# Optimization experiments

Hardware: AMD Instinct MI355X
Metric: run time of the kernel (lower is better)

## Reference

```python
import math
import jax, jax.numpy as jnp
import numpy as np

NUM_HEADS = 16

def setup_inputs() -> dict:
    key = jax.random.key(0)
    k1, k2, k3, k4, k5 = jax.random.split(key, 5)
    B, S, D = 8, 4096, 1024
    x = jax.random.normal(k1, (B, S, D), dtype=jnp.float32)
    W_qkv = jax.random.normal(k2, (D, 3 * D), dtype=jnp.float32) * (1.0 / math.sqrt(D))
    b_qkv = jax.random.normal(k3, (3 * D,), dtype=jnp.float32) * 0.02
    W_out = jax.random.normal(k4, (D, D), dtype=jnp.float32) * (1.0 / math.sqrt(D))
    b_out = jax.random.normal(k5, (D,), dtype=jnp.float32) * 0.02
    return {"x": x, "W_qkv": W_qkv, "b_qkv": b_qkv, "W_out": W_out, "b_out": b_out}

def reference(x, W_qkv, b_qkv, W_out, b_out):
    B, S, D = x.shape
    H = NUM_HEADS
    hd = D // H
    scale = 1.0 / math.sqrt(hd)
    # QKV projection: (B,S,D) -> (B,S,3D), reshaped to (B,S,H,3*hd)
    qkv = (x @ W_qkv + b_qkv).reshape(B, S, H, 3 * hd)
    q, k, v = jnp.split(qkv, 3, axis=-1)  # each (B,S,H,hd)
    # Faithful to source: no head permute, so attention is across the H heads
    # at each (batch, seq) position. scores: (B,S,H,H)
    scores = jnp.einsum('bsqd,bskd->bsqk', q, k) * scale
    attn = jax.nn.softmax(scores, axis=-1)
    values = jnp.einsum('bsqk,bskd->bsqd', attn, v).reshape(B, S, D)
    return values @ W_out + b_out
```

## Files before the change

kernel.cpp:

```cpp
#include <hip/hip_runtime.h>
#include <hip/hip_bf16.h>

#define TOKENS   32768
#define DMODEL   1024
#define THREE_D  3072

using u16 = unsigned short;
typedef __attribute__((ext_vector_type(8))) short short8;
typedef __attribute__((ext_vector_type(4))) float f32x4;

__device__ __forceinline__ float bf2f(u16 u) {
  union { unsigned int i; float f; } v; v.i = ((unsigned int)u) << 16; return v.f;
}
__device__ __forceinline__ u16 f2bf(float f) {
  __hip_bfloat16 h = __float2bfloat16(f);
  return *reinterpret_cast<u16*>(&h);
}

__device__ __forceinline__ void gload_lds16(const u16* g, u16* l) {
  __builtin_amdgcn_global_load_lds((const __attribute__((address_space(1))) void*)g,
                                   (__attribute__((address_space(3))) void*)l,
                                   16, 0, 0);
}

__global__ __launch_bounds__(256) void convert_f32_bf16(const float* __restrict__ in,
                                                        u16* __restrict__ out, long n) {
  long i = ((long)blockIdx.x * 256 + threadIdx.x) * 4;
  if (i >= n) return;
  float4 v = *reinterpret_cast<const float4*>(in + i);
  ushort4 o;
  o.x = f2bf(v.x); o.y = f2bf(v.y); o.z = f2bf(v.z); o.w = f2bf(v.w);
  *reinterpret_cast<ushort4*>(out + i) = o;
}

__global__ __launch_bounds__(256) void transpose_convert(const float* __restrict__ in,
                                                         u16* __restrict__ out,
                                                         int R, int C) {
  __shared__ u16 tile[32][33];
  const int bc = blockIdx.x * 32;
  const int br = blockIdx.y * 32;
  const int tx = threadIdx.x & 31;
  const int ty = threadIdx.x >> 5;
  #pragma unroll
  for (int i = 0; i < 32; i += 8)
    tile[ty + i][tx] = f2bf(in[(long)(br + ty + i) * C + bc + tx]);
  __syncthreads();
  #pragma unroll
  for (int i = 0; i < 32; i += 8)
    out[(long)(bc + ty + i) * R + br + tx] = tile[tx][ty + i];
}

#define BM 128
#define BN 128
#define BK 64

template <bool OUT_F32>
__global__ __launch_bounds__(256) void gemm_bt_bias(
    const u16* __restrict__ A, const u16* __restrict__ BT,
    const float* __restrict__ bias, void* __restrict__ Cv,
    int M, int N, int K, long a_stride, int a_grp) {
  __shared__ alignas(16) u16 As[BM * BK];
  __shared__ alignas(16) u16 Bs[BN * BK];

  const int tiles_n = N / BN;
  const int bm = (blockIdx.x / tiles_n) * BM;
  const int bn = (blockIdx.x % tiles_n) * BN;
  const int tid  = threadIdx.x;
  const int wave = tid >> 6;
  const int lane = tid & 63;
  const int wm   = (wave & 1) * 64;
  const int wn   = (wave >> 1) * 64;
  const int lrow = lane & 15;
  const int quad = lane >> 4;

  const int sr     = lane >> 3;
  const int schunk = (lane & 7) ^ sr;
  const int scol   = schunk * 8;

  f32x4 acc[4][4];
  #pragma unroll
  for (int i = 0; i < 4; i++)
    #pragma unroll
    for (int j = 0; j < 4; j++) acc[i][j] = (f32x4){0.f, 0.f, 0.f, 0.f};

  for (int k0 = 0; k0 < K; k0 += BK) {
    const long aoff = (long)(k0 >> 6) * a_grp + scol;
    __syncthreads();
    #pragma unroll
    for (int r = 0; r < 4; r++) {
      const int row = wave * 32 + r * 8 + sr;
      gload_lds16(A  + (long)(bm + row) * a_stride + aoff, As + (wave * 32 + r * 8) * BK);
      gload_lds16(BT + (long)(bn + row) * K + k0 + scol,  Bs + (wave * 32 + r * 8) * BK);
    }
    __syncthreads();

    #pragma unroll
    for (int kh = 0; kh < 2; kh++) {
      const int xs = lrow & 7;
      short8 a[4], b[4];
      #pragma unroll
      for (int mi = 0; mi < 4; mi++)
        a[mi] = *reinterpret_cast<const short8*>(
            &As[(wm + mi * 16 + lrow) * BK + (((kh * 4 + quad) ^ xs) * 8)]);
      #pragma unroll
      for (int ni = 0; ni < 4; ni++)
        b[ni] = *reinterpret_cast<const short8*>(
            &Bs[(wn + ni * 16 + lrow) * BK + (((kh * 4 + quad) ^ xs) * 8)]);
      #pragma unroll
      for (int mi = 0; mi < 4; mi++)
        #pragma unroll
        for (int ni = 0; ni < 4; ni++)
          acc[mi][ni] = __builtin_amdgcn_mfma_f32_16x16x32_bf16(a[mi], b[ni], acc[mi][ni], 0, 0, 0);
    }
  }

  #pragma unroll
  for (int ni = 0; ni < 4; ni++) {
    const int col = bn + wn + ni * 16 + lrow;
    const float bv = bias[col];
    #pragma unroll
    for (int mi = 0; mi < 4; mi++) {
      #pragma unroll
      for (int r = 0; r < 4; r++) {
        const int row = bm + wm + mi * 16 + (lane >> 4) * 4 + r;
        const float val = acc[mi][ni][r] + bv;
        if (OUT_F32)
          ((float*)Cv)[(long)row * N + col] = val;
        else
          ((u16*)Cv)[(long)row * N + col] = f2bf(val);
      }
    }
  }
}

__global__ __launch_bounds__(256) void attn_local(u16* __restrict__ qkv) {
  __shared__ float p_s[4][16][16];
  const int tid  = threadIdx.x;
  const int wave = tid >> 6;
  const int lane = tid & 63;
  const int t    = blockIdx.x * 4 + wave;
  u16* row = qkv + (long)t * THREE_D;
  const int lrow = lane & 15;
  const int quad = lane >> 4;
  const int kq   = quad * 8;

  short8 a0 = *reinterpret_cast<const short8*>(row + lrow * 192 + kq);
  short8 a1 = *reinterpret_cast<const short8*>(row + lrow * 192 + 32 + kq);
  short8 b0 = *reinterpret_cast<const short8*>(row + lrow * 192 + 64 + kq);
  short8 b1 = *reinterpret_cast<const short8*>(row + lrow * 192 + 96 + kq);
  f32x4 s = {0.f, 0.f, 0.f, 0.f};
  s = __builtin_amdgcn_mfma_f32_16x16x32_bf16(a0, b0, s, 0, 0, 0);
  s = __builtin_amdgcn_mfma_f32_16x16x32_bf16(a1, b1, s, 0, 0, 0);

  const float scale = 0.125f;
  float p[4];
  #pragma unroll
  for (int r = 0; r < 4; r++) {
    float x = s[r] * scale;
    float m = x;
    #pragma unroll
    for (int mask = 1; mask < 16; mask <<= 1) m = fmaxf(m, __shfl_xor(m, mask));
    float e = __expf(x - m);
    float l = e;
    #pragma unroll
    for (int mask = 1; mask < 16; mask <<= 1) l += __shfl_xor(l, mask);
    p[r] = e / l;
  }
  #pragma unroll
  for (int r = 0; r < 4; r++) p_s[wave][quad * 4 + r][lrow] = p[r];
  __syncthreads();

  float o[16];
  #pragma unroll
  for (int i = 0; i < 16; i++) o[i] = 0.f;
  #pragma unroll
  for (int j = 0; j < 16; j++) {
    float vj = bf2f(row[j * 192 + 128 + lane]);
    #pragma unroll
    for (int i = 0; i < 16; i++) o[i] += p_s[wave][i][j] * vj;
  }
  #pragma unroll
  for (int i = 0; i < 16; i++)
    row[i * 192 + lane] = f2bf(o[i]);
}

extern "C" void kernel_launch(void* const* d_in, const int* in_sizes, int n_in,
                              void* d_out, int out_size, void* d_ws, size_t ws_size,
                              hipStream_t stream) {
  const float* x     = (const float*)d_in[0];
  const float* W_qkv = (const float*)d_in[1];
  const float* b_qkv = (const float*)d_in[2];
  const float* W_out = (const float*)d_in[3];
  const float* b_out = (const float*)d_in[4];
  float* out = (float*)d_out;

  char* ws = (char*)d_ws;
  u16* qkv   = (u16*)ws;  ws += (size_t)TOKENS * THREE_D * 2;
  u16* x_bf  = (u16*)ws;  ws += (size_t)TOKENS * DMODEL * 2;
  u16* wqkvT = (u16*)ws;  ws += (size_t)THREE_D * DMODEL * 2;
  u16* woutT = (u16*)ws;

  dim3 tb(256);
  convert_f32_bf16<<<dim3((TOKENS * DMODEL) / 1024), tb, 0, stream>>>(
      x, x_bf, (long)TOKENS * DMODEL);
  transpose_convert<<<dim3(THREE_D / 32, DMODEL / 32), tb, 0, stream>>>(W_qkv, wqkvT, DMODEL, THREE_D);
  transpose_convert<<<dim3(DMODEL / 32, DMODEL / 32), tb, 0, stream>>>(W_out, woutT, DMODEL, DMODEL);
  gemm_bt_bias<false><<<dim3((TOKENS / BM) * (THREE_D / BN)), tb, 0, stream>>>(
      x_bf, wqkvT, b_qkv, qkv, TOKENS, THREE_D, DMODEL, (long)DMODEL, 64);
  attn_local<<<dim3(TOKENS / 4), tb, 0, stream>>>(qkv);
  gemm_bt_bias<true><<<dim3((TOKENS / BM) * (DMODEL / BN)), tb, 0, stream>>>(
      qkv, woutT, b_out, out, TOKENS, DMODEL, DMODEL, (long)THREE_D, 192);
}
```

Measured before the change: 643.3 us.

## Rewrite GEMM as 256x256 double-buffered 8-wave pipelined kernel with XCD remap

Replaces the 128x128 single-buffered GEMM with a 256x256 tile computed by 512 threads. It uses double-buffered LDS and splits each k-step into quadrant phases, staging the next half-tiles while MFMAs run, with explicit vmcnt waits, barriers and setprio. It also remaps block IDs across the 8 XCDs for better L2 locality. The aim is to hide global-load latency and raise data reuse per tile, at the cost of more LDS use, more registers and fragile hand-ordered synchronisation.

```diff
diff --git a/kernel.cpp b/kernel.cpp
--- a/kernel.cpp
+++ b/kernel.cpp
@@ -50,84 +50,147 @@
     out[(long)(bc + ty + i) * R + br + tx] = tile[tx][ty + i];
 }
 
-#define BM 128
-#define BN 128
+#define BM 256
+#define BN 256
 #define BK 64
 
+#define VM4 asm volatile("s_waitcnt vmcnt(4)" ::: "memory")
+#define VM0 asm volatile("s_waitcnt vmcnt(0)" ::: "memory")
+#define VMN ((void)0)
+#define NOSTAGE ((void)0)
+
+#define STAGE_A(T, H)                                                          \
+  { _Pragma("unroll") for (int j_ = 0; j_ < 2; j_++) {                         \
+      const int lr_ = (H) * 128 + (wave * 2 + j_) * 8;                         \
+      gload_lds16(A + (long)(bm + lr_ + sr) * a_stride + (long)(T) * a_grp + scol, \
+                  &As[(T) & 1][lr_ * BK]);                                     \
+  } }
+#define STAGE_B(T, H)                                                          \
+  { _Pragma("unroll") for (int j_ = 0; j_ < 2; j_++) {                         \
+      const int lr_ = (H) * 128 + (wave * 2 + j_) * 8;                         \
+      gload_lds16(BT + (long)(bn + lr_ + sr) * K + (T) * BK + scol,            \
+                  &Bs[(T) & 1][lr_ * BK]);                                     \
+  } }
+
+#define PHASE(BUF, QR, QC, RDA, STAGE, VMW)                                    \
+  {                                                                            \
+    if (RDA) {                                                                 \
+      _Pragma("unroll") for (int mi = 0; mi < 2; mi++)                         \
+        _Pragma("unroll") for (int kh = 0; kh < 2; kh++)                       \
+          a[mi][kh] = *reinterpret_cast<const short8*>(                        \
+              &As[BUF][((QR) * 128 + wrow + mi * 16 + lrow) * BK +             \
+                       (((kh * 4 + quad) ^ xs) * 8)]);                         \
+    }                                                                          \
+    short8 b[4][2];                                                            \
+    _Pragma("unroll") for (int ni = 0; ni < 4; ni++)                           \
+      _Pragma("unroll") for (int kh = 0; kh < 2; kh++)                         \
+        b[ni][kh] = *reinterpret_cast<const short8*>(                          \
+            &Bs[BUF][((QC) * 128 + wcol + ni * 16 + lrow) * BK +               \
+                     (((kh * 4 + quad) ^ xs) * 8)]);                           \
+    STAGE;                                                                     \
+    VMW;                                                                       \
+    __builtin_amdgcn_s_barrier();                                              \
+    asm volatile("s_waitcnt lgkmcnt(0)" ::: "memory");                         \
+    __builtin_amdgcn_sched_barrier(0);                                         \
+    __builtin_amdgcn_s_setprio(1);                                             \
+    _Pragma("unroll") for (int mi = 0; mi < 2; mi++)                           \
+      _Pragma("unroll") for (int ni = 0; ni < 4; ni++) {                       \
+        acc[QR][QC][mi][ni] = __builtin_amdgcn_mfma_f32_16x16x32_bf16(         \
+            a[mi][0], b[ni][0], acc[QR][QC][mi][ni], 0, 0, 0);                 \
+        acc[QR][QC][mi][ni] = __builtin_amdgcn_mfma_f32_16x16x32_bf16(         \
+            a[mi][1], b[ni][1], acc[QR][QC][mi][ni], 0, 0, 0);                 \
+      }                                                                        \
+    __builtin_amdgcn_s_setprio(0);                                             \
+    __builtin_amdgcn_s_barrier();                                              \
+    __builtin_amdgcn_sched_barrier(0);                                         \
+  }
+
 template <bool OUT_F32>
-__global__ __launch_bounds__(256) void gemm_bt_bias(
+__global__ __launch_bounds__(512, 2) void gemm_bt_bias(
     const u16* __restrict__ A, const u16* __restrict__ BT,
     const float* __restrict__ bias, void* __restrict__ Cv,
     int M, int N, int K, long a_stride, int a_grp) {
-  __shared__ alignas(16) u16 As[BM * BK];
-  __shared__ alignas(16) u16 Bs[BN * BK];
-
+  __shared__ alignas(16) u16 As[2][BM * BK];
+  __shared__ alignas(16) u16 Bs[2][BN * BK];
+  (void)M;
+
+  const int cpx = gridDim.x >> 3;
+  const int wg  = ((int)blockIdx.x & 7) * cpx + ((int)blockIdx.x >> 3);
   const int tiles_n = N / BN;
-  const int bm = (blockIdx.x / tiles_n) * BM;
-  const int bn = (blockIdx.x % tiles_n) * BN;
+  const int bm = (wg / tiles_n) * BM;
+  const int bn = (wg % tiles_n) * BN;
+
   const int tid  = threadIdx.x;
   const int wave = tid >> 6;
   const int lane = tid & 63;
-  const int wm   = (wave & 1) * 64;
-  const int wn   = (wave >> 1) * 64;
+  const int wrow = (wave & 3) * 32;
+  const int wcol = (wave >> 2) * 64;
   const int lrow = lane & 15;
   const int quad = lane >> 4;
+  const int xs   = lrow & 7;
 
   const int sr     = lane >> 3;
   const int schunk = (lane & 7) ^ sr;
   const int scol   = schunk * 8;
 
-  f32x4 acc[4][4];
-  #pragma unroll
-  for (int i = 0; i < 4; i++)
-    #pragma unroll
-    for (int j = 0; j < 4; j++) acc[i][j] = (f32x4){0.f, 0.f, 0.f, 0.f};
-
-  for (int k0 = 0; k0 < K; k0 += BK) {
-    const long aoff = (long)(k0 >> 6) * a_grp + scol;
-    __syncthreads();
-    #pragma unroll
-    for (int r = 0; r < 4; r++) {
-      const int row = wave * 32 + r * 8 + sr;
-      gload_lds16(A  + (long)(bm + row) * a_stride + aoff, As + (wave * 32 + r * 8) * BK);
-      gload_lds16(BT + (long)(bn + row) * K + k0 + scol,  Bs + (wave * 32 + r * 8) * BK);
-    }
-    __syncthreads();
-
-    #pragma unroll
-    for (int kh = 0; kh < 2; kh++) {
-      const int xs = lrow & 7;
-      short8 a[4], b[4];
+  const int NT = K / BK;
+
+  f32x4 acc[2][2][2][4];
+  #pragma unroll
+  for (int i = 0; i < 2; i++)
+    #pragma unroll
+    for (int j = 0; j < 2; j++)
       #pragma unroll
-      for (int mi = 0; mi < 4; mi++)
-        a[mi] = *reinterpret_cast<const short8*>(
-            &As[(wm + mi * 16 + lrow) * BK + (((kh * 4 + quad) ^ xs) * 8)]);
+      for (int m = 0; m < 2; m++)
+        #pragma unroll
+        for (int n = 0; n < 4; n++) acc[i][j][m][n] = (f32x4){0.f, 0.f, 0.f, 0.f};
+
+  STAGE_A(0, 0); STAGE_A(0, 1); STAGE_B(0, 0); STAGE_B(0, 1);
+  STAGE_A(1, 0); STAGE_B(1, 1);
+  VM4;
+  __builtin_amdgcn_s_barrier();
+
+  short8 a[2][2];
+  #pragma unroll 1
+  for (int t = 0; t + 2 < NT; t += 2) {
+    PHASE(0, 0, 0, 1, STAGE_A(t + 1, 1), VMN);
+    PHASE(0, 0, 1, 0, STAGE_B(t + 1, 0), VMN);
+    PHASE(0, 1, 1, 1, STAGE_A(t + 2, 0), VMN);
+    PHASE(0, 1, 0, 0, STAGE_B(t + 2, 1), VM4);
+    PHASE(1, 0, 0, 1, STAGE_A(t + 2, 1), VMN);
+    PHASE(1, 0, 1, 0, STAGE_B(t + 2, 0), VMN);
+    PHASE(1, 1, 1, 1, STAGE_A(t + 3, 0), VMN);
+    PHASE(1, 1, 0, 0, STAGE_B(t + 3, 1), VM4);
+  }
+  PHASE(0, 0, 0, 1, STAGE_A(NT - 1, 1), VMN);
+  PHASE(0, 0, 1, 0, STAGE_B(NT - 1, 0), VMN);
+  PHASE(0, 1, 1, 1, NOSTAGE, VMN);
+  PHASE(0, 1, 0, 0, NOSTAGE, VM0);
+  PHASE(1, 0, 0, 1, NOSTAGE, VMN);
+  PHASE(1, 0, 1, 0, NOSTAGE, VMN);
+  PHASE(1, 1, 1, 1, NOSTAGE, VMN);
+  PHASE(1, 1, 0, 0, NOSTAGE, VMN);
+
+  #pragma unroll
+  for (int qc = 0; qc < 2; qc++) {
+    #pragma unroll
+    for (int ni = 0; ni < 4; ni++) {
+      const int col = bn + qc * 128 + wcol + ni * 16 + lrow;
+      const float bv = bias[col];
       #pragma unroll
-      for (int ni = 0; ni < 4; ni++)
-        b[ni] = *reinterpret_cast<const short8*>(
-            &Bs[(wn + ni * 16 + lrow) * BK + (((kh * 4 + quad) ^ xs) * 8)]);
-      #pragma unroll
-      for (int mi = 0; mi < 4; mi++)
+      for (int qr = 0; qr < 2; qr++) {
         #pragma unroll
-        for (int ni = 0; ni < 4; ni++)
-          acc[mi][ni] = __builtin_amdgcn_mfma_f32_16x16x32_bf16(a[mi], b[ni], acc[mi][ni], 0, 0, 0);
-    }
-  }
-
-  #pragma unroll
-  for (int ni = 0; ni < 4; ni++) {
-    const int col = bn + wn + ni * 16 + lrow;
-    const float bv = bias[col];
-    #pragma unroll
-    for (int mi = 0; mi < 4; mi++) {
-      #pragma unroll
-      for (int r = 0; r < 4; r++) {
-        const int row = bm + wm + mi * 16 + (lane >> 4) * 4 + r;
-        const float val = acc[mi][ni][r] + bv;
-        if (OUT_F32)
-          ((float*)Cv)[(long)row * N + col] = val;
-        else
-          ((u16*)Cv)[(long)row * N + col] = f2bf(val);
+        for (int mi = 0; mi < 2; mi++) {
+          #pragma unroll
+          for (int r = 0; r < 4; r++) {
+            const int row = bm + qr * 128 + wrow + mi * 16 + quad * 4 + r;
+            const float val = acc[qr][qc][mi][ni][r] + bv;
+            if (OUT_F32)
+              ((float*)Cv)[(long)row * N + col] = val;
+            else
+              ((u16*)Cv)[(long)row * N + col] = f2bf(val);
+          }
+        }
       }
     }
   }
@@ -201,13 +264,14 @@
   u16* woutT = (u16*)ws;
 
   dim3 tb(256);
+  dim3 gtb(512);
   convert_f32_bf16<<<dim3((TOKENS * DMODEL) / 1024), tb, 0, stream>>>(
       x, x_bf, (long)TOKENS * DMODEL);
   transpose_convert<<<dim3(THREE_D / 32, DMODEL / 32), tb, 0, stream>>>(W_qkv, wqkvT, DMODEL, THREE_D);
   transpose_convert<<<dim3(DMODEL / 32, DMODEL / 32), tb, 0, stream>>>(W_out, woutT, DMODEL, DMODEL);
-  gemm_bt_bias<false><<<dim3((TOKENS / BM) * (THREE_D / BN)), tb, 0, stream>>>(
+  gemm_bt_bias<false><<<dim3((TOKENS / BM) * (THREE_D / BN)), gtb, 0, stream>>>(
       x_bf, wqkvT, b_qkv, qkv, TOKENS, THREE_D, DMODEL, (long)DMODEL, 64);
   attn_local<<<dim3(TOKENS / 4), tb, 0, stream>>>(qkv);
-  gemm_bt_bias<true><<<dim3((TOKENS / BM) * (DMODEL / BN)), tb, 0, stream>>>(
+  gemm_bt_bias<true><<<dim3((TOKENS / BM) * (DMODEL / BN)), gtb, 0, stream>>>(
       qkv, woutT, b_out, out, TOKENS, DMODEL, DMODEL, (long)THREE_D, 192);
 }
```

New measurement: 612.0 us. 1.05x faster.
